# Kernel tuning notes

Hardware: AMD Instinct MI355X
Metric: run time of the kernel (lower is better)

The kernel has to match this reference:

```python
import jax, jax.numpy as jnp
import numpy as np
from jax import lax

NUM_SAMPLE_POINTS = 1024
BIG = jnp.float32(1e10)  # stands in for +inf, fp16-safe


def setup_inputs() -> dict:
    key = jax.random.key(0)
    input = jax.random.normal(key, (8, 65536, 3), dtype=jnp.float32)
    return {"input": input}


def _fps_indices(points, num_samples):
    # points: [B, N, 3] -> indices [B, num_samples] int32
    B, N, _ = points.shape

    def step(carry, _):
        min_dist, farthest = carry  # [B, N], [B]
        cur = jnp.take_along_axis(points, farthest[:, None, None], axis=1)  # [B,1,3]
        d = jnp.sum((points - cur) ** 2, axis=-1)  # [B, N] squared distances
        min_dist = jnp.minimum(min_dist, d)
        nxt = jnp.argmax(min_dist, axis=-1).astype(jnp.int32)  # [B]
        return (min_dist, nxt), farthest

    init = (jnp.full((B, N), BIG, dtype=points.dtype), jnp.zeros((B,), jnp.int32))
    _, idx = lax.scan(step, init, None, length=num_samples)  # idx: [M, B]
    return idx.T  # [B, M]


def reference(input):
    # Faithful FPS: iteratively pick the point farthest from the selected set,
    # starting from index 0 (standard PointNet++ convention).
    idx = _fps_indices(input, NUM_SAMPLE_POINTS)  # [B, M] int32
    sampled = jnp.take_along_axis(input, idx[:, :, None], axis=1)  # [B, M, 3]
    return idx, sampled
```

## Files before the change

kernel.cpp:

```cpp
#include <hip/hip_runtime.h>


#define NB    8
#define NPTS  65536
#define NSAMP 1024
#define WPB   8
#define TPB   1024
#define PPT   8
#define RECQ  16

typedef unsigned long long ull;

#define DPP(x, ctrl) \
  ((unsigned)__builtin_amdgcn_update_dpp((int)(x), (int)(x), (ctrl), 0xf, 0xf, false))

__device__ __forceinline__ unsigned umax_wave64(unsigned x) {
  unsigned t;
  t = DPP(x, 0x111); x = t > x ? t : x;
  t = DPP(x, 0x112); x = t > x ? t : x;
  t = DPP(x, 0x114); x = t > x ? t : x;
  t = DPP(x, 0x118); x = t > x ? t : x;
  t = DPP(x, 0x142); x = t > x ? t : x;
  t = DPP(x, 0x143); x = t > x ? t : x;
  return (unsigned)__builtin_amdgcn_readlane((int)x, 63);
}
__device__ __forceinline__ unsigned umax_row16(unsigned x) {
  unsigned t;
  t = DPP(x, 0x111); x = t > x ? t : x;
  t = DPP(x, 0x112); x = t > x ? t : x;
  t = DPP(x, 0x114); x = t > x ? t : x;
  t = DPP(x, 0x118); x = t > x ? t : x;
  return (unsigned)__builtin_amdgcn_readlane((int)x, 15);
}
__device__ __forceinline__ unsigned umax_low8(unsigned x) {
  unsigned t;
  t = DPP(x, 0x111); x = t > x ? t : x;
  t = DPP(x, 0x112); x = t > x ? t : x;
  t = DPP(x, 0x114); x = t > x ? t : x;
  return (unsigned)__builtin_amdgcn_readlane((int)x, 7);
}

__device__ __forceinline__ void ld3_sc0(const ull* p, ull& a, ull& b, ull& c) {
  asm volatile(
      "global_load_dwordx2 %0, %3, off sc0\n\t"
      "global_load_dwordx2 %1, %3, off offset:8 sc0\n\t"
      "global_load_dwordx2 %2, %3, off offset:16 sc0\n\t"
      "s_waitcnt vmcnt(0)"
      : "=&v"(a), "=&v"(b), "=&v"(c) : "v"(p) : "memory");
}
__device__ __forceinline__ void st3_sc0(ull* p, ull a, ull b, ull c) {
  asm volatile(
      "global_store_dwordx2 %3, %0, off sc0\n\t"
      "global_store_dwordx2 %3, %1, off offset:8 sc0\n\t"
      "global_store_dwordx2 %3, %2, off offset:16 sc0"
      :: "v"(a), "v"(b), "v"(c), "v"(p) : "memory");
}

__device__ __forceinline__ void stage2_pack(const unsigned red[16][5], int lane,
                                            ull tag, ull& w0, ull& w1, ull& w2,
                                            int& ewin) {
  const int e = lane & 15;
  const unsigned d2 = red[e][0];
  const unsigned nn = red[e][1];
  const unsigned mx = umax_row16(d2);
  const ull bb = __ballot(d2 == mx) & 0xFFFFull;
  if (__popcll(bb) == 1) {
    ewin = __ffsll(bb) - 1;
  } else {
    const unsigned v = (d2 == mx) ? (65535u - nn) : 0u;
    const unsigned mv = umax_row16(v);
    const ull b2 = __ballot((d2 == mx) && (v == mv)) & 0xFFFFull;
    ewin = __ffsll(b2) - 1;
  }
  const ull k2 = ((ull)d2 << 16) | (ull)(65535u - nn);
  const unsigned xb = red[e][2], yb = red[e][3], zb = red[e][4];
  w0 = (k2 << 16) | tag;
  w1 = ((ull)xb << 32) | ((ull)(yb >> 16) << 16) | tag;
  w2 = ((ull)(yb & 0xFFFFu) << 48) | ((ull)zb << 16) | tag;
}

__global__ __launch_bounds__(TPB, 4)
void fps_kernel(const float* __restrict__ pts, float* __restrict__ out,
                ull* __restrict__ ws) {
  const int wg   = blockIdx.x;
  const int b    = wg >> 3;
  const int w    = wg & 7;
  const int tid  = threadIdx.x;
  const int lane = tid & 63;
  const int wave = tid >> 6;

  const float* p = pts + (size_t)b * NPTS * 3;

  float px[PPT], py[PPT], pz[PPT], md[PPT];
#pragma unroll
  for (int i = 0; i < PPT; ++i) {
    const int n = w * (TPB * PPT) + i * TPB + tid;
    px[i] = p[3 * n + 0];
    py[i] = p[3 * n + 1];
    pz[i] = p[3 * n + 2];
    md[i] = 1e10f;
  }

  float cx = p[0], cy = p[1], cz = p[2];

  ull* baseL = ws + (size_t)b * (2 * WPB * RECQ);
  ull* baseI = ws + (size_t)NB * (2 * WPB * RECQ) + (size_t)b * (2 * WPB * RECQ);

  float* out_idx = out + (size_t)b * NSAMP;
  float* out_smp = out + (size_t)NB * NSAMP + (size_t)b * NSAMP * 3;

  if (w == 0 && tid == 0) {
    out_idx[0] = 0.0f;
    out_smp[0] = cx; out_smp[1] = cy; out_smp[2] = cz;
  }

  __shared__ unsigned red[16][5];
  __shared__ float bc[3];
  __shared__ int cnt;
  __shared__ int flag;

  if (tid == 0) { cnt = 0; flag = 0; }
  __syncthreads();

  bool useIF = false;

  for (int t = 0; t < NSAMP - 1; ++t) {
    float bv = -1.0f; int bi = 0; float bx = 0.f, by = 0.f, bz = 0.f;
#pragma unroll
    for (int i = 0; i < PPT; ++i) {
      const float dx = __fsub_rn(px[i], cx);
      const float dy = __fsub_rn(py[i], cy);
      const float dz = __fsub_rn(pz[i], cz);
      const float d  = __fadd_rn(__fadd_rn(__fmul_rn(dx, dx), __fmul_rn(dy, dy)),
                                 __fmul_rn(dz, dz));
      const float m = fminf(md[i], d);
      md[i] = m;
      if (m > bv) {
        bv = m; bi = i;
        bx = px[i]; by = py[i]; bz = pz[i];
      }
    }

    const unsigned dbits = __float_as_uint(bv);
    const unsigned mw = umax_wave64(dbits);
    const bool tied = (dbits == mw);
    const ull bal0 = __ballot(tied);
    int wlane;
    if (__popcll(bal0) == 1) {
      wlane = __ffsll(bal0) - 1;
    } else {
      ull sel = 0;
#pragma unroll
      for (int ii = 0; ii < PPT; ++ii) {
        const ull bb = __ballot(tied && (bi == ii));
        const bool take = (sel == 0) && (bb != 0);
        sel = take ? bb : sel;
      }
      wlane = __ffsll(sel) - 1;
    }
    if (lane == wlane) {
      red[wave][0] = dbits;
      red[wave][1] = (unsigned)(w * (TPB * PPT) + bi * TPB + tid);
      red[wave][2] = __float_as_uint(bx);
      red[wave][3] = __float_as_uint(by);
      red[wave][4] = __float_as_uint(bz);
    }

    const ull tag = (ull)(unsigned)(t + 1);
    const int par = t & 1;

    int ret = 0;
    if (lane == 0)
      ret = __hip_atomic_fetch_add(&cnt, 1, __ATOMIC_ACQ_REL,
                                   __HIP_MEMORY_SCOPE_WORKGROUP);
    const int isLast = __shfl((int)(ret == 16 * t + 15), 0, 64);
    if (isLast) {
      ull w0, w1, w2; int ewin;
      stage2_pack(red, lane, tag, w0, w1, w2, ewin);
      if (lane == ewin)
        st3_sc0(baseL + (size_t)(par * WPB + w) * RECQ, w0, w1, w2);
    }

    if (wave == 0) {
      const size_t roff = (size_t)(par * WPB + (lane & 7)) * RECQ;
      const ull* recL = baseL + roff;
      const ull* recI = baseI + roff;
      const bool mine = (lane < WPB);
      bool done = !mine;
      ull r0 = 0, r1 = 0, r2 = 0;
      int spins = 0;
      for (;;) {
        if (!done) {
          if (!useIF) {
            ld3_sc0(recL, r0, r1, r2);
          } else {
            r0 = __hip_atomic_load(recI + 0, __ATOMIC_RELAXED, __HIP_MEMORY_SCOPE_AGENT);
            r1 = __hip_atomic_load(recI + 1, __ATOMIC_RELAXED, __HIP_MEMORY_SCOPE_AGENT);
            r2 = __hip_atomic_load(recI + 2, __ATOMIC_RELAXED, __HIP_MEMORY_SCOPE_AGENT);
          }
          done = ((r0 & 0xFFFFull) == tag) & ((r1 & 0xFFFFull) == tag) &
                 ((r2 & 0xFFFFull) == tag);
          if (!done && !useIF && ++spins > 256) useIF = true;
        }
        if (__all(done)) break;
        if (useIF) __builtin_amdgcn_s_sleep(1);
      }

      const unsigned d3  = (unsigned)(r0 >> 32);
      const unsigned lnv = (unsigned)((r0 >> 16) & 0xFFFFull);
      const unsigned m3 = umax_low8(d3);
      const ull b3 = __ballot(d3 == m3) & 0xFFull;
      int src;
      if (__popcll(b3) == 1) {
        src = __ffsll(b3) - 1;
      } else {
        const unsigned v = (d3 == m3) ? lnv : 0u;
        const unsigned mv = umax_low8(v);
        const ull b4 = __ballot((d3 == m3) && (v == mv)) & 0xFFull;
        src = __ffsll(b4) - 1;
      }
      const float xx = __uint_as_float((unsigned)(r1 >> 32));
      const float yy = __uint_as_float(((unsigned)((r1 >> 16) & 0xFFFFull) << 16) |
                                       (unsigned)(r2 >> 48));
      const float zz = __uint_as_float((unsigned)((r2 >> 16) & 0xFFFFFFFFull));
      const int n2   = 65535 - (int)__shfl((int)lnv, src, 64);
      const float wx = __shfl(xx, src, 64);
      const float wy = __shfl(yy, src, 64);
      const float wz = __shfl(zz, src, 64);
      if (lane == 0) {
        bc[0] = wx; bc[1] = wy; bc[2] = wz;
        __hip_atomic_store(&flag, t + 1, __ATOMIC_RELEASE,
                           __HIP_MEMORY_SCOPE_WORKGROUP);
        if (w == 0) {
          out_idx[t + 1] = (float)n2;
          out_smp[(t + 1) * 3 + 0] = wx;
          out_smp[(t + 1) * 3 + 1] = wy;
          out_smp[(t + 1) * 3 + 2] = wz;
        }
      }
      cx = wx; cy = wy; cz = wz;
    } else {
      if (wave == 15) {
        while (__hip_atomic_load(&cnt, __ATOMIC_ACQUIRE,
                                 __HIP_MEMORY_SCOPE_WORKGROUP) < 16 * (t + 1)) {}
        ull w0, w1, w2; int ewin;
        stage2_pack(red, lane, tag, w0, w1, w2, ewin);
        if (lane == ewin) {
          ull* recI = baseI + (size_t)(par * WPB + w) * RECQ;
          __hip_atomic_store(recI + 0, w0, __ATOMIC_RELAXED, __HIP_MEMORY_SCOPE_AGENT);
          __hip_atomic_store(recI + 1, w1, __ATOMIC_RELAXED, __HIP_MEMORY_SCOPE_AGENT);
          __hip_atomic_store(recI + 2, w2, __ATOMIC_RELAXED, __HIP_MEMORY_SCOPE_AGENT);
        }
      }
      while (__hip_atomic_load(&flag, __ATOMIC_ACQUIRE,
                               __HIP_MEMORY_SCOPE_WORKGROUP) < t + 1) {}
      cx = bc[0]; cy = bc[1]; cz = bc[2];
    }
  }
}

extern "C" void kernel_launch(void* const* d_in, const int* in_sizes, int n_in,
                              void* d_out, int out_size, void* d_ws, size_t ws_size,
                              hipStream_t stream) {
  (void)in_sizes; (void)n_in; (void)out_size; (void)ws_size;
  const float* pts = (const float*)d_in[0];
  float* out = (float*)d_out;
  ull* ws = (ull*)d_ws;
  fps_kernel<<<dim3(NB * WPB), dim3(TPB), 0, stream>>>(pts, out, ws);
}
```

Baseline: 2.630 ms.

## Replace atomic counter and flag spin-waits with workgroup barriers in FPS loop

After: 2.374 ms. 1.11x faster.

```diff
diff --git a/kernel.cpp b/kernel.cpp
--- a/kernel.cpp
+++ b/kernel.cpp
@@ -116,11 +116,7 @@
 
   __shared__ unsigned red[16][5];
   __shared__ float bc[3];
-  __shared__ int cnt;
-  __shared__ int flag;
-
-  if (tid == 0) { cnt = 0; flag = 0; }
-  __syncthreads();
+  __shared__ int bn2;
 
   bool useIF = false;
 
@@ -165,23 +161,22 @@
       red[wave][3] = __float_as_uint(by);
       red[wave][4] = __float_as_uint(bz);
     }
+    __syncthreads();
 
     const ull tag = (ull)(unsigned)(t + 1);
     const int par = t & 1;
 
-    int ret = 0;
-    if (lane == 0)
-      ret = __hip_atomic_fetch_add(&cnt, 1, __ATOMIC_ACQ_REL,
-                                   __HIP_MEMORY_SCOPE_WORKGROUP);
-    const int isLast = __shfl((int)(ret == 16 * t + 15), 0, 64);
-    if (isLast) {
+    if (wave == 1) {
       ull w0, w1, w2; int ewin;
       stage2_pack(red, lane, tag, w0, w1, w2, ewin);
-      if (lane == ewin)
+      if (lane == ewin) {
         st3_sc0(baseL + (size_t)(par * WPB + w) * RECQ, w0, w1, w2);
-    }
-
-    if (wave == 0) {
+        ull* recI = baseI + (size_t)(par * WPB + w) * RECQ;
+        __hip_atomic_store(recI + 0, w0, __ATOMIC_RELAXED, __HIP_MEMORY_SCOPE_AGENT);
+        __hip_atomic_store(recI + 1, w1, __ATOMIC_RELAXED, __HIP_MEMORY_SCOPE_AGENT);
+        __hip_atomic_store(recI + 2, w2, __ATOMIC_RELAXED, __HIP_MEMORY_SCOPE_AGENT);
+      }
+    } else if (wave == 0) {
       const size_t roff = (size_t)(par * WPB + (lane & 7)) * RECQ;
       const ull* recL = baseL + roff;
       const ull* recI = baseI + roff;
@@ -228,34 +223,19 @@
       const float wy = __shfl(yy, src, 64);
       const float wz = __shfl(zz, src, 64);
       if (lane == 0) {
-        bc[0] = wx; bc[1] = wy; bc[2] = wz;
-        __hip_atomic_store(&flag, t + 1, __ATOMIC_RELEASE,
-                           __HIP_MEMORY_SCOPE_WORKGROUP);
-        if (w == 0) {
-          out_idx[t + 1] = (float)n2;
-          out_smp[(t + 1) * 3 + 0] = wx;
-          out_smp[(t + 1) * 3 + 1] = wy;
-          out_smp[(t + 1) * 3 + 2] = wz;
-        }
-      }
-      cx = wx; cy = wy; cz = wz;
-    } else {
-      if (wave == 15) {
-        while (__hip_atomic_load(&cnt, __ATOMIC_ACQUIRE,
-                                 __HIP_MEMORY_SCOPE_WORKGROUP) < 16 * (t + 1)) {}
-        ull w0, w1, w2; int ewin;
-        stage2_pack(red, lane, tag, w0, w1, w2, ewin);
-        if (lane == ewin) {
-          ull* recI = baseI + (size_t)(par * WPB + w) * RECQ;
-          __hip_atomic_store(recI + 0, w0, __ATOMIC_RELAXED, __HIP_MEMORY_SCOPE_AGENT);
-          __hip_atomic_store(recI + 1, w1, __ATOMIC_RELAXED, __HIP_MEMORY_SCOPE_AGENT);
-          __hip_atomic_store(recI + 2, w2, __ATOMIC_RELAXED, __HIP_MEMORY_SCOPE_AGENT);
-        }
-      }
-      while (__hip_atomic_load(&flag, __ATOMIC_ACQUIRE,
-                               __HIP_MEMORY_SCOPE_WORKGROUP) < t + 1) {}
-      cx = bc[0]; cy = bc[1]; cz = bc[2];
-    }
+        bc[0] = wx; bc[1] = wy; bc[2] = wz; bn2 = n2;
+      }
+    }
+    __syncthreads();
+
+    if (w == 0 && wave == 2 && lane == 0) {
+      const float wx = bc[0], wy = bc[1], wz = bc[2];
+      out_idx[t + 1] = (float)bn2;
+      out_smp[(t + 1) * 3 + 0] = wx;
+      out_smp[(t + 1) * 3 + 1] = wy;
+      out_smp[(t + 1) * 3 + 2] = wz;
+    }
+    cx = bc[0]; cy = bc[1]; cz = bc[2];
   }
 }
 
```
